# Performance work log

Measured on AMD Instinct MI355X. Metric: run time of the kernel, lower is better.

Reference implementation:

```python
import jax, jax.numpy as jnp
import numpy as np

N, E, D, H, C, TD, MD = 50000, 500000, 128, 2, 64, 32, 64


def setup_inputs() -> dict:
    key = jax.random.key(0)
    ks = jax.random.split(key, 16)
    s = 0.05
    return {
        "x": jax.random.normal(ks[0], (N, D), jnp.float32),
        "edge_index": jax.random.randint(ks[1], (2, E), 0, N, dtype=jnp.int64),
        "edge_time": jax.random.randint(ks[2], (E,), 0, 86400, dtype=jnp.int64),
        "msg": jax.random.normal(ks[3], (E, MD), jnp.float32),
        "Wt": jax.random.normal(ks[4], (1, TD), jnp.float32) * s,
        "bt": jax.random.normal(ks[5], (TD,), jnp.float32) * s,
        "Wq": jax.random.normal(ks[6], (D, H * C), jnp.float32) * s,
        "bq": jax.random.normal(ks[7], (H * C,), jnp.float32) * s,
        "Wk": jax.random.normal(ks[8], (D, H * C), jnp.float32) * s,
        "bk": jax.random.normal(ks[9], (H * C,), jnp.float32) * s,
        "Wv": jax.random.normal(ks[10], (D, H * C), jnp.float32) * s,
        "bv": jax.random.normal(ks[11], (H * C,), jnp.float32) * s,
        "We": jax.random.normal(ks[12], (TD + MD, H * C), jnp.float32) * s,
        "Wskip": jax.random.normal(ks[13], (D, H * C), jnp.float32) * s,
        "bskip": jax.random.normal(ks[14], (H * C,), jnp.float32) * s,
    }


def reference(x, edge_index, edge_time, msg, Wt, bt, Wq, bq, Wk, bk, Wv, bv, We, Wskip, bskip):
    n = x.shape[0]
    src, dst = edge_index[0], edge_index[1]

    # TGN-style time encoding: cos(Linear(t))  -> [E, TD]
    t = edge_time.astype(x.dtype)[:, None]
    rel_t = jnp.cos(t @ Wt + bt)
    edge_attr = jnp.concatenate([rel_t, msg], axis=-1)  # [E, TD+MD]

    # TransformerConv projections, reshaped to [n, H, C] then gathered per edge
    q = (x @ Wq + bq).reshape(n, H, C)[dst]   # [E, H, C]
    k = (x @ Wk + bk).reshape(n, H, C)[src]   # [E, H, C]
    v = (x @ Wv + bv).reshape(n, H, C)[src]   # [E, H, C]
    e = (edge_attr @ We).reshape(-1, H, C)    # [E, H, C]

    k = k + e
    alpha = (q * k).sum(-1) / jnp.sqrt(jnp.asarray(C, x.dtype))  # [E, H]

    # segment softmax over incoming edges of each dst node
    amax = jax.ops.segment_max(alpha, dst, num_segments=n)       # [n, H]
    amax = jnp.where(jnp.isfinite(amax), amax, 0.0)
    ex = jnp.exp(alpha - amax[dst])
    denom = jax.ops.segment_sum(ex, dst, num_segments=n)
    alpha = ex / (denom[dst] + 1e-16)                            # [E, H]

    out_e = (v + e) * alpha[..., None]                           # [E, H, C]
    out = jax.ops.segment_sum(out_e, dst, num_segments=n).reshape(n, H * C)

    # root/skip connection
    out = out + x @ Wskip + bskip
    return out
```

## Files before the change

kernel.cpp:

```cpp
#include <hip/hip_runtime.h>
#include <hip/hip_bf16.h>

#define NN 50000
#define NE 500000
#define DD 128
#define HCC 128
#define TDD 32
#define MDD 64

typedef __hip_bfloat16 bf16;
typedef _Float16 f16;
typedef __attribute__((ext_vector_type(8))) _Float16 f16x8;
typedef __attribute__((ext_vector_type(2))) _Float16 f16x2;
typedef __attribute__((ext_vector_type(4))) float f32x4;

__device__ __forceinline__ float2 bf2x(unsigned u) {
    union { unsigned v; float f; } a, b;
    a.v = u << 16; b.v = u & 0xffff0000u;
    float2 r; r.x = a.f; r.y = b.f; return r;
}

__global__ __launch_bounds__(256) void conv_x_kernel(
    const float* __restrict__ x, f16* __restrict__ xh)
{
    int i = blockIdx.x * 256 + threadIdx.x;
    if (i >= NN * DD / 4) return;
    float4 v = ((const float4*)x)[i];
    f16 o[4] = { (f16)v.x, (f16)v.y, (f16)v.z, (f16)v.w };
    *(uint2*)&xh[(size_t)i * 4] = *(uint2*)o;
}

__global__ __launch_bounds__(256) void conv_w_kernel(
    const float* __restrict__ Wq, const float* __restrict__ Wk,
    const float* __restrict__ Wv, const float* __restrict__ Wsk,
    const float* __restrict__ We,
    f16* __restrict__ WTh, f16* __restrict__ Weh, int* __restrict__ cnt)
{
    int idx = blockIdx.x * 256 + threadIdx.x;
    if (idx < 512 * 128) {
        int n = idx >> 7, k = idx & 127;
        int mat = n >> 7, col = n & 127;
        const float* W = (mat == 0) ? Wq : (mat == 1) ? Wk : (mat == 2) ? Wv : Wsk;
        WTh[idx] = (f16)W[k * 128 + col];
    } else if (idx < 512 * 128 + 96 * 128) {
        int i = idx - 512 * 128;
        Weh[i] = (f16)We[i];
    } else if (idx < 512 * 128 + 96 * 128 + NN) {
        cnt[idx - (512 * 128 + 96 * 128)] = 0;
    }
}

__global__ __launch_bounds__(256) void node_proj_kernel(
    const f16* __restrict__ xh, const f16* __restrict__ WTh,
    const float* __restrict__ bq, const float* __restrict__ bk,
    const float* __restrict__ bv, const float* __restrict__ bsk,
    f16* __restrict__ qh, f16* __restrict__ kh, f16* __restrict__ vh,
    float* __restrict__ outp)
{
    __shared__ f16 xs[64 * 136];
    __shared__ f16 ws[128 * 136];

    const int node0 = blockIdx.x * 64;
    const int g = blockIdx.y;

    for (int i = threadIdx.x; i < 64 * 32; i += 256) {
        int node = i >> 5, koff = (i & 31) * 4;
        int gn = node0 + node;
        uint2 val = {0u, 0u};
        if (gn < NN) val = *(const uint2*)&xh[(size_t)gn * DD + koff];
        *(uint2*)&xs[node * 136 + koff] = val;
    }
    const f16* wt = WTh + (size_t)g * 128 * 128;
    for (int i = threadIdx.x; i < 128 * 32; i += 256) {
        int n = i >> 5, koff = (i & 31) * 4;
        *(uint2*)&ws[n * 136 + koff] = *(const uint2*)&wt[n * 128 + koff];
    }
    __syncthreads();

    const int wave = threadIdx.x >> 6;
    const int lane = threadIdx.x & 63;
    const int m0 = wave * 16;
    const int lrow = lane & 15;
    const int lk = (lane >> 4) * 8;

    f32x4 acc[8];
    #pragma unroll
    for (int t = 0; t < 8; t++) acc[t] = (f32x4){0.f, 0.f, 0.f, 0.f};

    #pragma unroll
    for (int kc = 0; kc < 4; kc++) {
        f16x8 a = *(const f16x8*)&xs[(m0 + lrow) * 136 + kc * 32 + lk];
        #pragma unroll
        for (int t = 0; t < 8; t++) {
            f16x8 b = *(const f16x8*)&ws[(t * 16 + lrow) * 136 + kc * 32 + lk];
            acc[t] = __builtin_amdgcn_mfma_f32_16x16x32_f16(a, b, acc[t], 0, 0, 0);
        }
    }

    const float* bias = (g == 0) ? bq : (g == 1) ? bk : (g == 2) ? bv : bsk;
    f16* outh = (g == 0) ? qh : (g == 1) ? kh : vh;

    #pragma unroll 1
    for (int t = 0; t < 8; t++) {
        int col = t * 16 + lrow;
        float bc = bias[col];
        #pragma unroll
        for (int r = 0; r < 4; r++) {
            int node = node0 + m0 + (lane >> 4) * 4 + r;
            if (node < NN) {
                float val = acc[t][r] + bc;
                if (g < 3) outh[(size_t)node * HCC + col] = (f16)val;
                else       outp[(size_t)node * HCC + col] = val;
            }
        }
    }
}

__global__ __launch_bounds__(256) void g_kernel(
    const f16* __restrict__ qh, const f16* __restrict__ Weh,
    bf16* __restrict__ G)
{
    __shared__ f16 qs[64 * 136];
    __shared__ f16 ws[96 * 136];

    const int node0 = blockIdx.x * 64;
    for (int i = threadIdx.x; i < 64 * 32; i += 256) {
        int node = i >> 5, koff = (i & 31) * 4;
        int gn = node0 + node;
        uint2 val = {0u, 0u};
        if (gn < NN) val = *(const uint2*)&qh[(size_t)gn * DD + koff];
        *(uint2*)&qs[node * 136 + koff] = val;
    }
    for (int i = threadIdx.x; i < 96 * 32; i += 256) {
        int j = i >> 5, koff = (i & 31) * 4;
        *(uint2*)&ws[j * 136 + koff] = *(const uint2*)&Weh[j * 128 + koff];
    }
    __syncthreads();

    const int wave = threadIdx.x >> 6;
    const int lane = threadIdx.x & 63;
    const int m0 = wave * 16;
    const int lrow = lane & 15;
    const int lk = (lane >> 4) * 8;

    f16x8 afr[4];
    #pragma unroll
    for (int hk = 0; hk < 4; hk++) {
        int h = hk >> 1, kc = hk & 1;
        afr[hk] = *(const f16x8*)&qs[(m0 + lrow) * 136 + h * 64 + kc * 32 + lk];
    }

    f32x4 acc[12];
    #pragma unroll
    for (int t = 0; t < 12; t++) acc[t] = (f32x4){0.f, 0.f, 0.f, 0.f};

    #pragma unroll
    for (int t = 0; t < 12; t++) {
        int h = (t < 6) ? 0 : 1;
        int jt = (t < 6) ? t : t - 6;
        #pragma unroll
        for (int kc = 0; kc < 2; kc++) {
            f16x8 b = *(const f16x8*)&ws[(jt * 16 + lrow) * 136 + h * 64 + kc * 32 + lk];
            acc[t] = __builtin_amdgcn_mfma_f32_16x16x32_f16(afr[h * 2 + kc], b, acc[t], 0, 0, 0);
        }
    }

    #pragma unroll 1
    for (int t = 0; t < 12; t++) {
        int h = (t < 6) ? 0 : 1;
        int jt = (t < 6) ? t : t - 6;
        int col = h * 96 + jt * 16 + lrow;
        #pragma unroll
        for (int r = 0; r < 4; r++) {
            int node = node0 + m0 + (lane >> 4) * 4 + r;
            if (node < NN) G[(size_t)node * 192 + col] = __float2bfloat16(acc[t][r]);
        }
    }
}

__global__ __launch_bounds__(256) void hist_kernel(
    const int* __restrict__ ei, int* __restrict__ cnt)
{
    int gid = blockIdx.x * 256 + threadIdx.x;
    if (gid < NE) atomicAdd(&cnt[ei[NE + gid]], 1);
}

__global__ __launch_bounds__(256) void scan_a_kernel(
    const int* __restrict__ cnt, int* __restrict__ bsum)
{
    __shared__ int red[256];
    int gid = blockIdx.x * 256 + threadIdx.x;
    red[threadIdx.x] = (gid < NN) ? cnt[gid] : 0;
    __syncthreads();
    for (int off = 128; off > 0; off >>= 1) {
        if (threadIdx.x < off) red[threadIdx.x] += red[threadIdx.x + off];
        __syncthreads();
    }
    if (threadIdx.x == 0) bsum[blockIdx.x] = red[0];
}

__global__ __launch_bounds__(256) void scan_b_kernel(
    const int* __restrict__ bsum, int* __restrict__ boff, int* __restrict__ seg)
{
    __shared__ int s[256];
    int t = threadIdx.x;
    s[t] = (t < 196) ? bsum[t] : 0;
    __syncthreads();
    if (t == 0) {
        int run = 0;
        for (int b = 0; b < 196; b++) { int v = s[b]; s[b] = run; run += v; }
        seg[NN] = NE;
    }
    __syncthreads();
    if (t < 196) boff[t] = s[t];
}

__global__ __launch_bounds__(256) void scan_c_kernel(
    const int* __restrict__ cnt, const int* __restrict__ boff,
    int* __restrict__ seg, int* __restrict__ cur)
{
    __shared__ int s[256];
    int gid = blockIdx.x * 256 + threadIdx.x;
    int v = (gid < NN) ? cnt[gid] : 0;
    s[threadIdx.x] = v;
    __syncthreads();
    for (int off = 1; off < 256; off <<= 1) {
        int t = (threadIdx.x >= off) ? s[threadIdx.x - off] : 0;
        __syncthreads();
        s[threadIdx.x] += t;
        __syncthreads();
    }
    int excl = s[threadIdx.x] - v + boff[blockIdx.x];
    if (gid < NN) { seg[gid] = excl; cur[gid] = excl; }
}

__global__ __launch_bounds__(256) void scatter_kernel(
    const int* __restrict__ ei, const int* __restrict__ et,
    int* __restrict__ cur, int* __restrict__ perm,
    int* __restrict__ esrc, int* __restrict__ edst, float* __restrict__ etim)
{
    int gid = blockIdx.x * 256 + threadIdx.x;
    if (gid < NE) {
        int d = ei[NE + gid];
        int pos = atomicAdd(&cur[d], 1);
        perm[pos] = gid;
        esrc[pos] = ei[gid];
        edst[pos] = d;
        etim[pos] = (float)et[gid];
    }
}

__global__ __launch_bounds__(256) void msg_gather_kernel(
    const float* __restrict__ msg, const int* __restrict__ perm,
    bf16* __restrict__ emsg)
{
    size_t idx = (size_t)blockIdx.x * 256 + threadIdx.x;
    if (idx >= (size_t)NE * 8) return;
    int i = (int)(idx >> 3);
    int c8 = (int)(idx & 7);
    const float4* row = (const float4*)(msg + ((size_t)perm[i] << 6));
    float4 v0 = row[c8 * 2];
    float4 v1 = row[c8 * 2 + 1];
    bf16 o[8] = { __float2bfloat16(v0.x), __float2bfloat16(v0.y),
                  __float2bfloat16(v0.z), __float2bfloat16(v0.w),
                  __float2bfloat16(v1.x), __float2bfloat16(v1.y),
                  __float2bfloat16(v1.z), __float2bfloat16(v1.w) };
    *(uint4*)&emsg[idx * 8] = *(uint4*)o;
}

__global__ __launch_bounds__(256) void score_kernel(
    const int* __restrict__ esrc, const int* __restrict__ edst,
    const float* __restrict__ etim,
    const bf16* __restrict__ emsg,
    const float* __restrict__ Wt, const float* __restrict__ bt,
    const f16* __restrict__ qh, const f16* __restrict__ kh,
    const bf16* __restrict__ G, float2* __restrict__ exv)
{
    __shared__ float wt_s[TDD], bt_s[TDD];
    if (threadIdx.x < TDD) {
        wt_s[threadIdx.x] = Wt[threadIdx.x];
        bt_s[threadIdx.x] = bt[threadIdx.x];
    }
    __syncthreads();

    int i = blockIdx.x * 256 + threadIdx.x;
    if (i >= NE) return;

    int src = esrc[i], dst = edst[i];
    float t = etim[i];

    union U16 { uint4 u; f16x2 h[4]; };
    const uint4* qp = (const uint4*)(qh + (size_t)dst * DD);
    const uint4* kp = (const uint4*)(kh + (size_t)src * DD);
    float qk0 = 0.f, qk1 = 0.f;
    #pragma unroll
    for (int c = 0; c < 8; c++) {
        U16 a, b; a.u = qp[c]; b.u = kp[c];
        #pragma unroll
        for (int j = 0; j < 4; j++) {
#if defined(__has_builtin) && __has_builtin(__builtin_amdgcn_fdot2)
            qk0 = __builtin_amdgcn_fdot2(a.h[j], b.h[j], qk0, false);
#else
            qk0 = fmaf((float)a.h[j][0], (float)b.h[j][0], qk0);
            qk0 = fmaf((float)a.h[j][1], (float)b.h[j][1], qk0);
#endif
        }
    }
    #pragma unroll
    for (int c = 8; c < 16; c++) {
        U16 a, b; a.u = qp[c]; b.u = kp[c];
        #pragma unroll
        for (int j = 0; j < 4; j++) {
#if defined(__has_builtin) && __has_builtin(__builtin_amdgcn_fdot2)
            qk1 = __builtin_amdgcn_fdot2(a.h[j], b.h[j], qk1, false);
#else
            qk1 = fmaf((float)a.h[j][0], (float)b.h[j][0], qk1);
            qk1 = fmaf((float)a.h[j][1], (float)b.h[j][1], qk1);
#endif
        }
    }

    const uint4* gp = (const uint4*)(G + (size_t)dst * 192);
    float u0 = 0.f, u1 = 0.f;

    #pragma unroll
    for (int c = 0; c < 4; c++) {
        uint4 g0 = gp[c], g1 = gp[12 + c];
        float cj[8];
        #pragma unroll
        for (int j = 0; j < 8; j++)
            cj[j] = __cosf(fmaf(t, wt_s[8 * c + j], bt_s[8 * c + j]));
        float2 p;
        p = bf2x(g0.x); u0 = fmaf(cj[0], p.x, u0); u0 = fmaf(cj[1], p.y, u0);
        p = bf2x(g0.y); u0 = fmaf(cj[2], p.x, u0); u0 = fmaf(cj[3], p.y, u0);
        p = bf2x(g0.z); u0 = fmaf(cj[4], p.x, u0); u0 = fmaf(cj[5], p.y, u0);
        p = bf2x(g0.w); u0 = fmaf(cj[6], p.x, u0); u0 = fmaf(cj[7], p.y, u0);
        p = bf2x(g1.x); u1 = fmaf(cj[0], p.x, u1); u1 = fmaf(cj[1], p.y, u1);
        p = bf2x(g1.y); u1 = fmaf(cj[2], p.x, u1); u1 = fmaf(cj[3], p.y, u1);
        p = bf2x(g1.z); u1 = fmaf(cj[4], p.x, u1); u1 = fmaf(cj[5], p.y, u1);
        p = bf2x(g1.w); u1 = fmaf(cj[6], p.x, u1); u1 = fmaf(cj[7], p.y, u1);
    }

    const uint4* mp = (const uint4*)(emsg + ((size_t)i << 6));
    #pragma unroll
    for (int c = 0; c < 8; c++) {
        uint4 mu = mp[c];
        uint4 g0 = gp[4 + c], g1 = gp[16 + c];
        float2 m0 = bf2x(mu.x), m1 = bf2x(mu.y), m2 = bf2x(mu.z), m3 = bf2x(mu.w);
        float2 p;
        p = bf2x(g0.x); u0 = fmaf(m0.x, p.x, u0); u0 = fmaf(m0.y, p.y, u0);
        p = bf2x(g0.y); u0 = fmaf(m1.x, p.x, u0); u0 = fmaf(m1.y, p.y, u0);
        p = bf2x(g0.z); u0 = fmaf(m2.x, p.x, u0); u0 = fmaf(m2.y, p.y, u0);
        p = bf2x(g0.w); u0 = fmaf(m3.x, p.x, u0); u0 = fmaf(m3.y, p.y, u0);
        p = bf2x(g1.x); u1 = fmaf(m0.x, p.x, u1); u1 = fmaf(m0.y, p.y, u1);
        p = bf2x(g1.y); u1 = fmaf(m1.x, p.x, u1); u1 = fmaf(m1.y, p.y, u1);
        p = bf2x(g1.z); u1 = fmaf(m2.x, p.x, u1); u1 = fmaf(m2.y, p.y, u1);
        p = bf2x(g1.w); u1 = fmaf(m3.x, p.x, u1); u1 = fmaf(m3.y, p.y, u1);
    }

    float2 ex;
    ex.x = __expf((qk0 + u0) * 0.125f);
    ex.y = __expf((qk1 + u1) * 0.125f);
    exv[i] = ex;
}

__global__ __launch_bounds__(256) void agg_kernel(
    const int* __restrict__ esrc, const float* __restrict__ etim,
    const bf16* __restrict__ emsg,
    const float* __restrict__ Wt, const float* __restrict__ bt,
    const f16* __restrict__ vh, const float2* __restrict__ exv,
    const int* __restrict__ seg,
    float* __restrict__ Sv, float* __restrict__ dnv,
    float* __restrict__ outp)
{
    __shared__ float wt_s[TDD], bt_s[TDD];
    if (threadIdx.x < TDD) {
        wt_s[threadIdx.x] = Wt[threadIdx.x];
        bt_s[threadIdx.x] = bt[threadIdx.x];
    }
    __syncthreads();

    const int lane = threadIdx.x & 63;
    const int gw = blockIdx.x * 4 + (threadIdx.x >> 6);
    const int NW = gridDim.x * 4;
    const bool half0 = (lane < 32);
    const float wtv = wt_s[lane & 31];
    const float btv = bt_s[lane & 31];
    const int mcol = half0 ? (32 + lane) : (lane - 32);

    for (int n = gw; n < NN; n += NW) {
        const int s0 = seg[n], s1 = seg[n + 1];

        float2 acc; acc.x = 0.f; acc.y = 0.f;
        float accd = 0.f;
        float s00 = 0.f, s01 = 0.f, s10 = 0.f, s11 = 0.f;

        int i = s0;
        #pragma unroll 1
        for (; i + 4 <= s1; i += 4) {
            int srcu[4]; float2 exu[4]; float ttu[4]; float mgu[4]; f16x2 vvu[4];
            #pragma unroll
            for (int u = 0; u < 4; u++) {
                srcu[u] = esrc[i + u];
                exu[u]  = exv[i + u];
                ttu[u]  = etim[i + u];
                mgu[u]  = __bfloat162float(emsg[((size_t)(i + u) << 6) + mcol]);
            }
            #pragma unroll
            for (int u = 0; u < 4; u++)
                vvu[u] = *(const f16x2*)&vh[(size_t)srcu[u] * HCC + 2 * lane];
            #pragma unroll
            for (int u = 0; u < 4; u++) {
                float cs = __cosf(fmaf(ttu[u], wtv, btv));
                float r0 = half0 ? cs : mgu[u];
                float r1 = half0 ? mgu[u] : 0.f;
                float exh = half0 ? exu[u].x : exu[u].y;
                acc.x = fmaf(exh, (float)vvu[u][0], acc.x);
                acc.y = fmaf(exh, (float)vvu[u][1], acc.y);
                accd += exh;
                s00 = fmaf(exu[u].x, r0, s00); s01 = fmaf(exu[u].x, r1, s01);
                s10 = fmaf(exu[u].y, r0, s10); s11 = fmaf(exu[u].y, r1, s11);
            }
        }
        #pragma unroll 1
        for (; i < s1; i++) {
            int src = esrc[i];
            float2 ex = exv[i];
            float tt = etim[i];
            float mg = __bfloat162float(emsg[((size_t)i << 6) + mcol]);
            f16x2 v2 = *(const f16x2*)&vh[(size_t)src * HCC + 2 * lane];
            float cs = __cosf(fmaf(tt, wtv, btv));
            float r0 = half0 ? cs : mg;
            float r1 = half0 ? mg : 0.f;
            float exh = half0 ? ex.x : ex.y;
            acc.x = fmaf(exh, (float)v2[0], acc.x);
            acc.y = fmaf(exh, (float)v2[1], acc.y);
            accd += exh;
            s00 = fmaf(ex.x, r0, s00); s01 = fmaf(ex.x, r1, s01);
            s10 = fmaf(ex.y, r0, s10); s11 = fmaf(ex.y, r1, s11);
        }

        float dn = accd + 1e-16f;
        size_t sb = (size_t)n * 192;
        Sv[sb + lane]      = s00;
        Sv[sb + 96 + lane] = s10;
        if (half0) {
            Sv[sb + 64 + lane]  = s01;
            Sv[sb + 160 + lane] = s11;
        }
        if ((lane & 31) == 0) dnv[n * 2 + (lane >> 5)] = accd;

        size_t nb = (size_t)n * HCC + 2 * lane;
        float2 sk = *(const float2*)&outp[nb];
        float2 o;
        o.x = acc.x / dn + sk.x;
        o.y = acc.y / dn + sk.y;
        *(float2*)&outp[nb] = o;
    }
}

__global__ __launch_bounds__(256) void epi_kernel(
    const float* __restrict__ Sv, const float* __restrict__ dnv,
    const float* __restrict__ We, float* __restrict__ outp)
{
    __shared__ float st[192 * 36];
    const int node0 = blockIdx.x * 32;
    for (int idx = threadIdx.x; idx < 32 * 192; idx += 256) {
        int n = idx / 192, c = idx - n * 192;
        int node = node0 + n;
        st[c * 36 + n] = (node < NN) ? Sv[(size_t)node * 192 + c] : 0.f;
    }
    __syncthreads();

    const int wave = threadIdx.x >> 6;
    const int lane = threadIdx.x & 63;
    const int nb = wave * 8;
    const int hoff = (lane < 32) ? 0 : 96;
    const float2* We2 = (const float2*)We;

    float a[8][2];
    #pragma unroll
    for (int n = 0; n < 8; n++) { a[n][0] = 0.f; a[n][1] = 0.f; }

    #pragma unroll 8
    for (int j = 0; j < 96; j++) {
        float2 w = We2[j * 64 + lane];
        const float* sr = &st[(hoff + j) * 36 + nb];
        float sv[8];
        *(float4*)&sv[0] = *(const float4*)sr;
        *(float4*)&sv[4] = *(const float4*)(sr + 4);
        #pragma unroll
        for (int n = 0; n < 8; n++) {
            a[n][0] = fmaf(sv[n], w.x, a[n][0]);
            a[n][1] = fmaf(sv[n], w.y, a[n][1]);
        }
    }

    #pragma unroll 1
    for (int n = 0; n < 8; n++) {
        int node = node0 + nb + n;
        if (node >= NN) break;
        float dn = dnv[node * 2 + (lane >> 5)] + 1e-16f;
        size_t b = (size_t)node * HCC + 2 * lane;
        float2 o = *(const float2*)&outp[b];
        o.x += a[n][0] / dn;
        o.y += a[n][1] / dn;
        *(float2*)&outp[b] = o;
    }
}

extern "C" void kernel_launch(void* const* d_in, const int* in_sizes, int n_in,
                              void* d_out, int out_size, void* d_ws, size_t ws_size,
                              hipStream_t stream) {
    const float* x   = (const float*)d_in[0];
    const int* ei    = (const int*)d_in[1];
    const int* et    = (const int*)d_in[2];
    const float* msg = (const float*)d_in[3];
    const float* Wt  = (const float*)d_in[4];
    const float* bt  = (const float*)d_in[5];
    const float* Wq  = (const float*)d_in[6];
    const float* bq  = (const float*)d_in[7];
    const float* Wk  = (const float*)d_in[8];
    const float* bk  = (const float*)d_in[9];
    const float* Wv  = (const float*)d_in[10];
    const float* bv  = (const float*)d_in[11];
    const float* We  = (const float*)d_in[12];
    const float* Wsk = (const float*)d_in[13];
    const float* bsk = (const float*)d_in[14];

    const size_t nf = (size_t)NN * HCC;
    f16* xh      = (f16*)d_ws;
    f16* qh      = xh + nf;
    f16* kh      = qh + nf;
    f16* vh      = kh + nf;
    f16* WTh     = vh + nf;
    f16* Weh     = WTh + 512 * 128;
    bf16* G      = (bf16*)(Weh + 96 * 128);
    bf16* emsg   = G + (size_t)NN * 192;
    float2* exv  = (float2*)(emsg + (size_t)NE * MDD);
    float* etim  = (float*)(exv + NE);
    float* Sv    = etim + NE;
    float* dnv   = Sv + (size_t)NN * 192;
    int* cnt     = (int*)(dnv + (size_t)NN * 2);
    int* seg     = cnt + NN;
    int* cur     = seg + NN + 1;
    int* perm    = cur + NN;
    int* esrc    = perm + NE;
    int* edst    = esrc + NE;
    int* bsum    = edst + NE;
    int* boff    = bsum + 256;
    size_t need  = (size_t)((char*)(boff + 256) - (char*)d_ws);
    if (ws_size < need) return;

    float* outp = (float*)d_out;

    conv_x_kernel<<<(NN * DD / 4 + 255) / 256, 256, 0, stream>>>(x, xh);
    conv_w_kernel<<<(512 * 128 + 96 * 128 + NN + 255) / 256, 256, 0, stream>>>(
        Wq, Wk, Wv, Wsk, We, WTh, Weh, cnt);
    dim3 npgrid((NN + 63) / 64, 4);
    node_proj_kernel<<<npgrid, 256, 0, stream>>>(
        xh, WTh, bq, bk, bv, bsk, qh, kh, vh, outp);
    g_kernel<<<(NN + 63) / 64, 256, 0, stream>>>(qh, Weh, G);
    hist_kernel<<<(NE + 255) / 256, 256, 0, stream>>>(ei, cnt);
    scan_a_kernel<<<196, 256, 0, stream>>>(cnt, bsum);
    scan_b_kernel<<<1, 256, 0, stream>>>(bsum, boff, seg);
    scan_c_kernel<<<196, 256, 0, stream>>>(cnt, boff, seg, cur);
    scatter_kernel<<<(NE + 255) / 256, 256, 0, stream>>>(
        ei, et, cur, perm, esrc, edst, etim);
    msg_gather_kernel<<<(int)(((size_t)NE * 8 + 255) / 256), 256, 0, stream>>>(
        msg, perm, emsg);
    score_kernel<<<(NE + 255) / 256, 256, 0, stream>>>(
        esrc, edst, etim, emsg, Wt, bt, qh, kh, G, exv);
    agg_kernel<<<3125, 256, 0, stream>>>(
        esrc, etim, emsg, Wt, bt, vh, exv, seg, Sv, dnv, outp);
    epi_kernel<<<(NN + 31) / 32, 256, 0, stream>>>(Sv, dnv, We, outp);
}
```

Measured before the change: 624.7 us.

## Fuse message gather into score kernel with 8 lanes per edge

Merges the message gather/bf16 conversion kernel with the attention score kernel. Each edge is now handled by 8 lanes that each load a slice of q, k, G and the message row, then reduce the partial dot products with xor shuffles. This removes one launch and the re-read of the bf16 message buffer, and spreads each edge's work across lanes so loads are more coalesced. In exchange, per-edge index loads are repeated across the 8 lanes, a shuffle reduction is added, and the message term now uses fp32 values instead of the bf16-rounded ones.

```diff
diff --git a/kernel.cpp b/kernel.cpp
--- a/kernel.cpp
+++ b/kernel.cpp
@@ -250,118 +250,103 @@
     }
 }
 
-__global__ __launch_bounds__(256) void msg_gather_kernel(
+__global__ __launch_bounds__(256) void edge_fused_kernel(
     const float* __restrict__ msg, const int* __restrict__ perm,
-    bf16* __restrict__ emsg)
-{
+    const int* __restrict__ esrc, const int* __restrict__ edst,
+    const float* __restrict__ etim,
+    const float* __restrict__ Wt, const float* __restrict__ bt,
+    const f16* __restrict__ qh, const f16* __restrict__ kh,
+    const bf16* __restrict__ G,
+    bf16* __restrict__ emsg, float2* __restrict__ exv)
+{
+    __shared__ float wt_s[TDD], bt_s[TDD];
+    if (threadIdx.x < TDD) {
+        wt_s[threadIdx.x] = Wt[threadIdx.x];
+        bt_s[threadIdx.x] = bt[threadIdx.x];
+    }
+    __syncthreads();
+
     size_t idx = (size_t)blockIdx.x * 256 + threadIdx.x;
     if (idx >= (size_t)NE * 8) return;
     int i = (int)(idx >> 3);
-    int c8 = (int)(idx & 7);
-    const float4* row = (const float4*)(msg + ((size_t)perm[i] << 6));
-    float4 v0 = row[c8 * 2];
-    float4 v1 = row[c8 * 2 + 1];
+    int sub = (int)(idx & 7);
+
+    int src = esrc[i], dst = edst[i];
+    float t = etim[i];
+    int pe = perm[i];
+
+    const float4* mrow = (const float4*)(msg + ((size_t)pe << 6));
+    float4 v0 = mrow[sub * 2];
+    float4 v1 = mrow[sub * 2 + 1];
     bf16 o[8] = { __float2bfloat16(v0.x), __float2bfloat16(v0.y),
                   __float2bfloat16(v0.z), __float2bfloat16(v0.w),
                   __float2bfloat16(v1.x), __float2bfloat16(v1.y),
                   __float2bfloat16(v1.z), __float2bfloat16(v1.w) };
-    *(uint4*)&emsg[idx * 8] = *(uint4*)o;
-}
-
-__global__ __launch_bounds__(256) void score_kernel(
-    const int* __restrict__ esrc, const int* __restrict__ edst,
-    const float* __restrict__ etim,
-    const bf16* __restrict__ emsg,
-    const float* __restrict__ Wt, const float* __restrict__ bt,
-    const f16* __restrict__ qh, const f16* __restrict__ kh,
-    const bf16* __restrict__ G, float2* __restrict__ exv)
-{
-    __shared__ float wt_s[TDD], bt_s[TDD];
-    if (threadIdx.x < TDD) {
-        wt_s[threadIdx.x] = Wt[threadIdx.x];
-        bt_s[threadIdx.x] = bt[threadIdx.x];
-    }
-    __syncthreads();
-
-    int i = blockIdx.x * 256 + threadIdx.x;
-    if (i >= NE) return;
-
-    int src = esrc[i], dst = edst[i];
-    float t = etim[i];
+    *(uint4*)&emsg[((size_t)i << 6) + sub * 8] = *(uint4*)o;
 
     union U16 { uint4 u; f16x2 h[4]; };
-    const uint4* qp = (const uint4*)(qh + (size_t)dst * DD);
-    const uint4* kp = (const uint4*)(kh + (size_t)src * DD);
-    float qk0 = 0.f, qk1 = 0.f;
-    #pragma unroll
-    for (int c = 0; c < 8; c++) {
-        U16 a, b; a.u = qp[c]; b.u = kp[c];
-        #pragma unroll
-        for (int j = 0; j < 4; j++) {
+    const f16* qrow = qh + (size_t)dst * DD;
+    const f16* krow = kh + (size_t)src * DD;
+    U16 q0, k0, q1, k1;
+    q0.u = *(const uint4*)(qrow + 8 * sub);
+    k0.u = *(const uint4*)(krow + 8 * sub);
+    q1.u = *(const uint4*)(qrow + 64 + 8 * sub);
+    k1.u = *(const uint4*)(krow + 64 + 8 * sub);
+    float s0 = 0.f, s1 = 0.f;
+    #pragma unroll
+    for (int j = 0; j < 4; j++) {
 #if defined(__has_builtin) && __has_builtin(__builtin_amdgcn_fdot2)
-            qk0 = __builtin_amdgcn_fdot2(a.h[j], b.h[j], qk0, false);
+        s0 = __builtin_amdgcn_fdot2(q0.h[j], k0.h[j], s0, false);
+        s1 = __builtin_amdgcn_fdot2(q1.h[j], k1.h[j], s1, false);
 #else
-            qk0 = fmaf((float)a.h[j][0], (float)b.h[j][0], qk0);
-            qk0 = fmaf((float)a.h[j][1], (float)b.h[j][1], qk0);
+        s0 = fmaf((float)q0.h[j][0], (float)k0.h[j][0], s0);
+        s0 = fmaf((float)q0.h[j][1], (float)k0.h[j][1], s0);
+        s1 = fmaf((float)q1.h[j][0], (float)k1.h[j][0], s1);
+        s1 = fmaf((float)q1.h[j][1], (float)k1.h[j][1], s1);
 #endif
-        }
-    }
-    #pragma unroll
-    for (int c = 8; c < 16; c++) {
-        U16 a, b; a.u = qp[c]; b.u = kp[c];
-        #pragma unroll
-        for (int j = 0; j < 4; j++) {
-#if defined(__has_builtin) && __has_builtin(__builtin_amdgcn_fdot2)
-            qk1 = __builtin_amdgcn_fdot2(a.h[j], b.h[j], qk1, false);
-#else
-            qk1 = fmaf((float)a.h[j][0], (float)b.h[j][0], qk1);
-            qk1 = fmaf((float)a.h[j][1], (float)b.h[j][1], qk1);
-#endif
-        }
-    }
-
-    const uint4* gp = (const uint4*)(G + (size_t)dst * 192);
-    float u0 = 0.f, u1 = 0.f;
-
-    #pragma unroll
-    for (int c = 0; c < 4; c++) {
-        uint4 g0 = gp[c], g1 = gp[12 + c];
-        float cj[8];
-        #pragma unroll
-        for (int j = 0; j < 8; j++)
-            cj[j] = __cosf(fmaf(t, wt_s[8 * c + j], bt_s[8 * c + j]));
+    }
+
+    const bf16* grow = G + (size_t)dst * 192;
+
+    uint2 gc0 = *(const uint2*)(grow + 4 * sub);
+    uint2 gc1 = *(const uint2*)(grow + 96 + 4 * sub);
+    float cj[4];
+    #pragma unroll
+    for (int j = 0; j < 4; j++)
+        cj[j] = __cosf(fmaf(t, wt_s[4 * sub + j], bt_s[4 * sub + j]));
+    {
         float2 p;
-        p = bf2x(g0.x); u0 = fmaf(cj[0], p.x, u0); u0 = fmaf(cj[1], p.y, u0);
-        p = bf2x(g0.y); u0 = fmaf(cj[2], p.x, u0); u0 = fmaf(cj[3], p.y, u0);
-        p = bf2x(g0.z); u0 = fmaf(cj[4], p.x, u0); u0 = fmaf(cj[5], p.y, u0);
-        p = bf2x(g0.w); u0 = fmaf(cj[6], p.x, u0); u0 = fmaf(cj[7], p.y, u0);
-        p = bf2x(g1.x); u1 = fmaf(cj[0], p.x, u1); u1 = fmaf(cj[1], p.y, u1);
-        p = bf2x(g1.y); u1 = fmaf(cj[2], p.x, u1); u1 = fmaf(cj[3], p.y, u1);
-        p = bf2x(g1.z); u1 = fmaf(cj[4], p.x, u1); u1 = fmaf(cj[5], p.y, u1);
-        p = bf2x(g1.w); u1 = fmaf(cj[6], p.x, u1); u1 = fmaf(cj[7], p.y, u1);
-    }
-
-    const uint4* mp = (const uint4*)(emsg + ((size_t)i << 6));
-    #pragma unroll
-    for (int c = 0; c < 8; c++) {
-        uint4 mu = mp[c];
-        uint4 g0 = gp[4 + c], g1 = gp[16 + c];
-        float2 m0 = bf2x(mu.x), m1 = bf2x(mu.y), m2 = bf2x(mu.z), m3 = bf2x(mu.w);
+        p = bf2x(gc0.x); s0 = fmaf(cj[0], p.x, s0); s0 = fmaf(cj[1], p.y, s0);
+        p = bf2x(gc0.y); s0 = fmaf(cj[2], p.x, s0); s0 = fmaf(cj[3], p.y, s0);
+        p = bf2x(gc1.x); s1 = fmaf(cj[0], p.x, s1); s1 = fmaf(cj[1], p.y, s1);
+        p = bf2x(gc1.y); s1 = fmaf(cj[2], p.x, s1); s1 = fmaf(cj[3], p.y, s1);
+    }
+
+    uint4 gm0 = *(const uint4*)(grow + 32 + 8 * sub);
+    uint4 gm1 = *(const uint4*)(grow + 128 + 8 * sub);
+    {
         float2 p;
-        p = bf2x(g0.x); u0 = fmaf(m0.x, p.x, u0); u0 = fmaf(m0.y, p.y, u0);
-        p = bf2x(g0.y); u0 = fmaf(m1.x, p.x, u0); u0 = fmaf(m1.y, p.y, u0);
-        p = bf2x(g0.z); u0 = fmaf(m2.x, p.x, u0); u0 = fmaf(m2.y, p.y, u0);
-        p = bf2x(g0.w); u0 = fmaf(m3.x, p.x, u0); u0 = fmaf(m3.y, p.y, u0);
-        p = bf2x(g1.x); u1 = fmaf(m0.x, p.x, u1); u1 = fmaf(m0.y, p.y, u1);
-        p = bf2x(g1.y); u1 = fmaf(m1.x, p.x, u1); u1 = fmaf(m1.y, p.y, u1);
-        p = bf2x(g1.z); u1 = fmaf(m2.x, p.x, u1); u1 = fmaf(m2.y, p.y, u1);
-        p = bf2x(g1.w); u1 = fmaf(m3.x, p.x, u1); u1 = fmaf(m3.y, p.y, u1);
-    }
-
-    float2 ex;
-    ex.x = __expf((qk0 + u0) * 0.125f);
-    ex.y = __expf((qk1 + u1) * 0.125f);
-    exv[i] = ex;
+        p = bf2x(gm0.x); s0 = fmaf(v0.x, p.x, s0); s0 = fmaf(v0.y, p.y, s0);
+        p = bf2x(gm0.y); s0 = fmaf(v0.z, p.x, s0); s0 = fmaf(v0.w, p.y, s0);
+        p = bf2x(gm0.z); s0 = fmaf(v1.x, p.x, s0); s0 = fmaf(v1.y, p.y, s0);
+        p = bf2x(gm0.w); s0 = fmaf(v1.z, p.x, s0); s0 = fmaf(v1.w, p.y, s0);
+        p = bf2x(gm1.x); s1 = fmaf(v0.x, p.x, s1); s1 = fmaf(v0.y, p.y, s1);
+        p = bf2x(gm1.y); s1 = fmaf(v0.z, p.x, s1); s1 = fmaf(v0.w, p.y, s1);
+        p = bf2x(gm1.z); s1 = fmaf(v1.x, p.x, s1); s1 = fmaf(v1.y, p.y, s1);
+        p = bf2x(gm1.w); s1 = fmaf(v1.z, p.x, s1); s1 = fmaf(v1.w, p.y, s1);
+    }
+
+    #pragma unroll
+    for (int off = 1; off < 8; off <<= 1) {
+        s0 += __shfl_xor(s0, off);
+        s1 += __shfl_xor(s1, off);
+    }
+    if (sub == 0) {
+        float2 ex;
+        ex.x = __expf(s0 * 0.125f);
+        ex.y = __expf(s1 * 0.125f);
+        exv[i] = ex;
+    }
 }
 
 __global__ __launch_bounds__(256) void agg_kernel(
@@ -567,10 +552,8 @@
     scan_c_kernel<<<196, 256, 0, stream>>>(cnt, boff, seg, cur);
     scatter_kernel<<<(NE + 255) / 256, 256, 0, stream>>>(
         ei, et, cur, perm, esrc, edst, etim);
-    msg_gather_kernel<<<(int)(((size_t)NE * 8 + 255) / 256), 256, 0, stream>>>(
-        msg, perm, emsg);
-    score_kernel<<<(NE + 255) / 256, 256, 0, stream>>>(
-        esrc, edst, etim, emsg, Wt, bt, qh, kh, G, exv);
+    edge_fused_kernel<<<(int)(((size_t)NE * 8 + 255) / 256), 256, 0, stream>>>(
+        msg, perm, esrc, edst, etim, Wt, bt, qh, kh, G, emsg, exv);
     agg_kernel<<<3125, 256, 0, stream>>>(
         esrc, etim, emsg, Wt, bt, vh, exv, seg, Sv, dnv, outp);
     epi_kernel<<<(NN + 31) / 32, 256, 0, stream>>>(Sv, dnv, We, outp);
```

Result: faster. 561.6 us (-10.1%).
